# Performance work log

Hardware: AMD Instinct MI355X
Metric: run time of the kernel (lower is better)

## Reference

```python
import jax, jax.numpy as jnp
import numpy as np

HEAD_DIM = 64
NUM_FEATURES = 256


def _sample_orf(head_dim, num_features, seed=0):
    """Orthogonal random features with chi(d)-norm row scaling (FAVOR+)."""
    rng = np.random.RandomState(seed)
    blocks = []
    while len(blocks) * head_dim < num_features:
        G = rng.randn(head_dim, head_dim).astype(np.float32)
        Q, _ = np.linalg.qr(G)
        norms = np.linalg.norm(rng.randn(head_dim, head_dim).astype(np.float32), axis=1)
        blocks.append(np.diag(norms) @ Q.T)
    return np.concatenate(blocks, axis=0)[:num_features].astype(np.float32)


def _phi(x, omega, is_query):
    """FAVOR+ positive feature map with max-subtraction stabilization."""
    m = omega.shape[0]
    proj = jnp.einsum('bhnd,md->bhnm', x, omega)          # [B,H,N,M]
    norm = 0.5 * jnp.sum(x * x, axis=-1, keepdims=True)    # [B,H,N,1]
    log_phi = proj - norm
    if is_query:
        log_phi = log_phi - jnp.max(log_phi, axis=-1, keepdims=True)
    else:
        log_phi = log_phi - jnp.max(log_phi)
    return jnp.exp(log_phi) / np.float32(np.sqrt(m)) + 1e-4


def _causal_scan(phi_q, phi_k, v):
    """Causal linear-attention recurrence via lax.scan. States: S[B,H,M,D], z[B,H,M]."""
    B, H, N, M = phi_q.shape
    D = v.shape[-1]
    # seq-first for scan: [N,B,H,*]
    pq = jnp.moveaxis(phi_q, 2, 0)
    pk = jnp.moveaxis(phi_k, 2, 0)
    vt = jnp.moveaxis(v, 2, 0)

    S0 = jnp.zeros((B, H, M, D), dtype=phi_q.dtype)
    z0 = jnp.zeros((B, H, M), dtype=phi_q.dtype)

    def step(carry, xs):
        S, z = carry
        pq_i, pk_i, v_i = xs  # [B,H,M], [B,H,M], [B,H,D]
        S = S + pk_i[..., :, None] * v_i[..., None, :]
        z = z + pk_i
        num = jnp.einsum('bhm,bhmd->bhd', pq_i, S)
        den = jnp.sum(pq_i * z, axis=-1, keepdims=True) + 1e-6
        return (S, z), num / den

    _, out = jax.lax.scan(step, (S0, z0), (pq, pk, vt))  # out: [N,B,H,D]
    return jnp.moveaxis(out, 0, 2)


def setup_inputs() -> dict:
    key = jax.random.key(0)
    k1, k2, k3 = jax.random.split(key, 3)
    B, H, N, D = 2, 16, 4096, HEAD_DIM
    q = jax.random.normal(k1, (B, H, N, D), dtype=jnp.float32)
    k = jax.random.normal(k2, (B, H, N, D), dtype=jnp.float32)
    v = jax.random.normal(k3, (B, H, N, D), dtype=jnp.float32)
    omega = jnp.asarray(_sample_orf(HEAD_DIM, NUM_FEATURES))
    return {"q": q, "k": k, "v": v, "omega": omega}


def reference(q, k, v, omega):
    scale = q.shape[-1] ** (-0.25)
    phi_q = _phi(q * scale, omega, is_query=True)
    phi_k = _phi(k * scale, omega, is_query=False)
    # q_len == kv_len -> causal scan branch (matches original forward)
    out = _causal_scan(phi_q.astype(jnp.float32), phi_k.astype(jnp.float32),
                       v.astype(jnp.float32))
    return out.astype(q.dtype)
```

## Files before the change

### kernel.cpp

```cpp
#include <hip/hip_runtime.h>
#include <cstddef>

#define BH    32
#define NSEQ  4096
#define MFEAT 256
#define CHUNK 128
#define NCH   32
#define SROW  65
#define SPITCH (SROW*256)

#define SCALE 0.35355339059327373f

typedef unsigned int uint_t;
typedef _Float16 half_t;
typedef __attribute__((ext_vector_type(8))) _Float16 half8;
typedef __attribute__((ext_vector_type(4))) float f32x4;

__device__ __forceinline__ f32x4 mfma16(half8 a, half8 b, f32x4 c) {
  return __builtin_amdgcn_mfma_f32_16x16x32_f16(a, b, c, 0, 0, 0);
}
__device__ __forceinline__ uint_t enc_f(float x) {
  uint_t u = __float_as_uint(x);
  return (u & 0x80000000u) ? ~u : (u | 0x80000000u);
}
__device__ __forceinline__ float dec_f(uint_t u) {
  u = (u & 0x80000000u) ? (u ^ 0x80000000u) : ~u;
  return __uint_as_float(u);
}
__device__ __forceinline__ half8 cvt_h8(float4 a, float4 b) {
  half8 h;
  h[0] = (half_t)a.x; h[1] = (half_t)a.y; h[2] = (half_t)a.z; h[3] = (half_t)a.w;
  h[4] = (half_t)b.x; h[5] = (half_t)b.y; h[6] = (half_t)b.z; h[7] = (half_t)b.w;
  return h;
}

__global__ void k_init(uint_t* kmax) { *kmax = enc_f(-__builtin_inff()); }

__global__ __launch_bounds__(256, 2) void k_maxes(
    const float* __restrict__ q, const float* __restrict__ kx,
    const float* __restrict__ omega, float* __restrict__ rowmQ,
    uint_t* __restrict__ kmax)
{
  __shared__ half_t Wl[256 * 72];
  __shared__ half_t xs[64 * 72];
  __shared__ float nrm[64];
  __shared__ float red[4];

  const int tid = threadIdx.x;
  const int lane = tid & 63;
  const int w = tid >> 6;
  const int lc = lane & 15, rg = lane >> 4, koff = rg * 8;
  const size_t rowbase = (size_t)blockIdx.x * 64;

  for (int l = tid; l < 4096; l += 256) {
    int m = l >> 4, d4 = (l & 15) * 4;
    float4 o = *(const float4*)(omega + m * 64 + d4);
    half_t* p = &Wl[m * 72 + d4];
    p[0] = (half_t)o.x; p[1] = (half_t)o.y; p[2] = (half_t)o.z; p[3] = (half_t)o.w;
  }
  {
    int r = tid >> 2, qd = tid & 3;
    #pragma unroll
    for (int c = 0; c < 4; c++) {
      float4 xv = *(const float4*)(q + (rowbase + r) * 64 + qd * 16 + c * 4);
      half_t* p = &xs[r * 72 + qd * 16 + c * 4];
      p[0] = (half_t)(xv.x * SCALE); p[1] = (half_t)(xv.y * SCALE);
      p[2] = (half_t)(xv.z * SCALE); p[3] = (half_t)(xv.w * SCALE);
    }
  }
  __syncthreads();
  {
    f32x4 acc[16];
    #pragma unroll
    for (int ct = 0; ct < 16; ct++) acc[ct] = (f32x4){0.f, 0.f, 0.f, 0.f};
    #pragma unroll
    for (int ks = 0; ks < 2; ks++) {
      half8 a = *(const half8*)&xs[(w * 16 + lc) * 72 + ks * 32 + koff];
      #pragma unroll
      for (int ct = 0; ct < 16; ct++) {
        half8 b = *(const half8*)&Wl[(ct * 16 + lc) * 72 + ks * 32 + koff];
        acc[ct] = mfma16(a, b, acc[ct]);
      }
    }
    #pragma unroll
    for (int r = 0; r < 4; r++) {
      float m0 = -3.4e38f;
      #pragma unroll
      for (int ct = 0; ct < 16; ct++) m0 = fmaxf(m0, acc[ct][r]);
      m0 = fmaxf(m0, __shfl_xor(m0, 1, 64));
      m0 = fmaxf(m0, __shfl_xor(m0, 2, 64));
      m0 = fmaxf(m0, __shfl_xor(m0, 4, 64));
      m0 = fmaxf(m0, __shfl_xor(m0, 8, 64));
      if (lc == 0) rowmQ[rowbase + w * 16 + rg * 4 + r] = m0;
    }
  }
  __syncthreads();
  {
    int r = tid >> 2, qd = tid & 3;
    float pn = 0.f;
    #pragma unroll
    for (int c = 0; c < 4; c++) {
      float4 xv = *(const float4*)(kx + (rowbase + r) * 64 + qd * 16 + c * 4);
      xv.x *= SCALE; xv.y *= SCALE; xv.z *= SCALE; xv.w *= SCALE;
      pn += xv.x * xv.x + xv.y * xv.y + xv.z * xv.z + xv.w * xv.w;
      half_t* p = &xs[r * 72 + qd * 16 + c * 4];
      p[0] = (half_t)xv.x; p[1] = (half_t)xv.y; p[2] = (half_t)xv.z; p[3] = (half_t)xv.w;
    }
    pn += __shfl_xor(pn, 1, 64);
    pn += __shfl_xor(pn, 2, 64);
    if ((tid & 3) == 0) nrm[r] = 0.5f * pn;
  }
  __syncthreads();
  {
    f32x4 acc[16];
    #pragma unroll
    for (int ct = 0; ct < 16; ct++) acc[ct] = (f32x4){0.f, 0.f, 0.f, 0.f};
    #pragma unroll
    for (int ks = 0; ks < 2; ks++) {
      half8 a = *(const half8*)&xs[(w * 16 + lc) * 72 + ks * 32 + koff];
      #pragma unroll
      for (int ct = 0; ct < 16; ct++) {
        half8 b = *(const half8*)&Wl[(ct * 16 + lc) * 72 + ks * 32 + koff];
        acc[ct] = mfma16(a, b, acc[ct]);
      }
    }
    float hn[4];
    #pragma unroll
    for (int r = 0; r < 4; r++) hn[r] = nrm[w * 16 + rg * 4 + r];
    float bm = -3.4e38f;
    #pragma unroll
    for (int ct = 0; ct < 16; ct++)
      #pragma unroll
      for (int r = 0; r < 4; r++) bm = fmaxf(bm, acc[ct][r] - hn[r]);
    #pragma unroll
    for (int off = 1; off < 64; off <<= 1) bm = fmaxf(bm, __shfl_xor(bm, off, 64));
    if (lane == 0) red[w] = bm;
    __syncthreads();
    if (tid == 0)
      atomicMax(kmax, enc_f(fmaxf(fmaxf(red[0], red[1]), fmaxf(red[2], red[3]))));
  }
}

__global__ __launch_bounds__(256, 2) void k_state(
    const float* __restrict__ kx, const float* __restrict__ v,
    const float* __restrict__ omega, const uint_t* __restrict__ kmax,
    half_t* __restrict__ spA)
{
  __shared__ half_t WP[256 * 72];
  __shared__ half_t vt[80 * 136];
  __shared__ float nrmK[128];

  const int tid = threadIdx.x;
  const int lane = tid & 63;
  const int w = tid >> 6;
  const int lc = lane & 15, rg = lane >> 4, koff = rg * 8;
  const int wr = w * 32;
  const int blk = blockIdx.x;
  const size_t nbase = (size_t)(blk >> 5) * NSEQ + (size_t)(blk & 31) * CHUNK;
  const float gmaxv = dec_f(*kmax);

  for (int l = tid; l < 4096; l += 256) {
    int m = l >> 4, d4 = (l & 15) * 4;
    float4 o = *(const float4*)(omega + m * 64 + d4);
    half_t* p = &WP[m * 72 + d4];
    p[0] = (half_t)o.x; p[1] = (half_t)o.y; p[2] = (half_t)o.z; p[3] = (half_t)o.w;
  }
  for (int l = tid; l < 2048; l += 256) {
    int j = l >> 4, dq = (l & 15) * 4;
    float4 vv = *(const float4*)(v + (nbase + j) * 64 + dq);
    vt[(dq + 0) * 136 + j] = (half_t)vv.x;
    vt[(dq + 1) * 136 + j] = (half_t)vv.y;
    vt[(dq + 2) * 136 + j] = (half_t)vv.z;
    vt[(dq + 3) * 136 + j] = (half_t)vv.w;
  }
  if (tid < 128) vt[64 * 136 + tid] = (half_t)1.0f;

  half8 ak[2][2];
  float pn[2] = {0.f, 0.f};
  #pragma unroll
  for (int rt = 0; rt < 2; rt++) {
    const float* kp = kx + (nbase + wr + rt * 16 + lc) * 64 + koff;
    #pragma unroll
    for (int ks = 0; ks < 2; ks++) {
      float4 a = *(const float4*)(kp + ks * 32);
      float4 b = *(const float4*)(kp + ks * 32 + 4);
      a.x *= SCALE; a.y *= SCALE; a.z *= SCALE; a.w *= SCALE;
      b.x *= SCALE; b.y *= SCALE; b.z *= SCALE; b.w *= SCALE;
      pn[rt] += a.x * a.x + a.y * a.y + a.z * a.z + a.w * a.w
              + b.x * b.x + b.y * b.y + b.z * b.z + b.w * b.w;
      ak[rt][ks] = cvt_h8(a, b);
    }
    pn[rt] += __shfl_xor(pn[rt], 16, 64);
    pn[rt] += __shfl_xor(pn[rt], 32, 64);
  }
  if (rg == 0) {
    nrmK[wr + lc] = 0.5f * pn[0];
    nrmK[wr + 16 + lc] = 0.5f * pn[1];
  }
  __syncthreads();

  f32x4 accP[2][16];
  #pragma unroll
  for (int rt = 0; rt < 2; rt++)
    #pragma unroll
    for (int ct = 0; ct < 16; ct++) accP[rt][ct] = (f32x4){0.f, 0.f, 0.f, 0.f};
  #pragma unroll
  for (int ks = 0; ks < 2; ks++)
    #pragma unroll
    for (int ct = 0; ct < 16; ct++) {
      half8 b = *(const half8*)&WP[(ct * 16 + lc) * 72 + ks * 32 + koff];
      accP[0][ct] = mfma16(ak[0][ks], b, accP[0][ct]);
      accP[1][ct] = mfma16(ak[1][ks], b, accP[1][ct]);
    }
  float hnr[2][4];
  #pragma unroll
  for (int rt = 0; rt < 2; rt++)
    #pragma unroll
    for (int r = 0; r < 4; r++) hnr[rt][r] = nrmK[wr + rt * 16 + rg * 4 + r];
  #pragma unroll
  for (int rt = 0; rt < 2; rt++)
    #pragma unroll
    for (int ct = 0; ct < 16; ct++)
      #pragma unroll
      for (int r = 0; r < 4; r++)
        accP[rt][ct][r] = __expf(accP[rt][ct][r] - hnr[rt][r] - gmaxv) * 0.0625f + 1e-4f;

  half_t* pkT = WP;
  #pragma unroll
  for (int h = 0; h < 2; h++) {
    __syncthreads();
    #pragma unroll
    for (int rt = 0; rt < 2; rt++)
      #pragma unroll
      for (int c8 = 0; c8 < 8; c8++) {
        int ct = h * 8 + c8;
        #pragma unroll
        for (int r = 0; r < 4; r++)
          pkT[(c8 * 16 + lc) * 144 + wr + rt * 16 + rg * 4 + r] = (half_t)accP[rt][ct][r];
      }
    __syncthreads();
    f32x4 acc2[5][2];
    #pragma unroll
    for (int rt = 0; rt < 5; rt++) {
      acc2[rt][0] = (f32x4){0.f, 0.f, 0.f, 0.f};
      acc2[rt][1] = (f32x4){0.f, 0.f, 0.f, 0.f};
    }
    #pragma unroll
    for (int ks = 0; ks < 4; ks++) {
      half8 b0 = *(const half8*)&pkT[((2 * w + 0) * 16 + lc) * 144 + ks * 32 + koff];
      half8 b1 = *(const half8*)&pkT[((2 * w + 1) * 16 + lc) * 144 + ks * 32 + koff];
      #pragma unroll
      for (int rt = 0; rt < 5; rt++) {
        half8 a = *(const half8*)&vt[(rt * 16 + lc) * 136 + ks * 32 + koff];
        acc2[rt][0] = mfma16(a, b0, acc2[rt][0]);
        acc2[rt][1] = mfma16(a, b1, acc2[rt][1]);
      }
    }
    #pragma unroll
    for (int rt = 0; rt < 5; rt++)
      #pragma unroll
      for (int c2 = 0; c2 < 2; c2++)
        #pragma unroll
        for (int r = 0; r < 4; r++) {
          int row = rt * 16 + rg * 4 + r;
          if (row < SROW)
            spA[(size_t)blk * SPITCH + row * 256 + h * 128 + (2 * w + c2) * 16 + lc] =
                (half_t)acc2[rt][c2][r];
        }
  }
}

__global__ __launch_bounds__(256) void k_prefix(
    const uint_t* __restrict__ spA, uint_t* __restrict__ spB)
{
  int r = blockIdx.x * 256 + threadIdx.x;
  if (r >= SPITCH / 2) return;
  int bh = blockIdx.y;
  const uint_t* src = spA + (size_t)bh * NCH * (SPITCH / 2) + r;
  uint_t* dst = spB + (size_t)bh * NCH * (SPITCH / 2) + r;
  float r0 = 0.f, r1 = 0.f;
  for (int c = 0; c < NCH; c++) {
    union { uint_t u; half_t h[2]; } cv, ov;
    cv.u = src[(size_t)c * (SPITCH / 2)];
    ov.h[0] = (half_t)r0; ov.h[1] = (half_t)r1;
    dst[(size_t)c * (SPITCH / 2)] = ov.u;
    r0 += (float)cv.h[0];
    r1 += (float)cv.h[1];
  }
}

__global__ __launch_bounds__(256, 2) void k_attn2(
    const float* __restrict__ q, const float* __restrict__ kx,
    const float* __restrict__ v, const float* __restrict__ omega,
    const float* __restrict__ rowmQ, const uint_t* __restrict__ kmax,
    const half_t* __restrict__ spB, float* __restrict__ out)
{
  __shared__ half_t sm[24192];
  __shared__ float nrmK[128];
  half_t* PQ  = sm;
  half_t* PK  = sm + 9216;
  half_t* SST = sm + 18432;
  half_t* AS  = sm;
  half_t* VT  = sm + 9216;

  const int tid = threadIdx.x;
  const int lane = tid & 63;
  const int w = tid >> 6;
  const int lc = lane & 15, rg = lane >> 4, koff = rg * 8;
  const int wr = w * 32;
  const int blk = blockIdx.x;
  const size_t nbase = (size_t)(blk >> 5) * NSEQ + (size_t)(blk & 31) * CHUNK;
  const half_t* spb = spB + (size_t)blk * SPITCH;
  const float gmaxv = dec_f(*kmax);

  float rowm[2][4];
  #pragma unroll
  for (int rt = 0; rt < 2; rt++)
    #pragma unroll
    for (int r = 0; r < 4; r++)
      rowm[rt][r] = rowmQ[nbase + wr + rt * 16 + rg * 4 + r];

  half8 aq[2][2], ak[2][2];
  float pn[2] = {0.f, 0.f};
  #pragma unroll
  for (int rt = 0; rt < 2; rt++) {
    const float* qp = q + (nbase + wr + rt * 16 + lc) * 64 + koff;
    const float* kp = kx + (nbase + wr + rt * 16 + lc) * 64 + koff;
    #pragma unroll
    for (int ks = 0; ks < 2; ks++) {
      float4 a = *(const float4*)(qp + ks * 32);
      float4 b = *(const float4*)(qp + ks * 32 + 4);
      a.x *= SCALE; a.y *= SCALE; a.z *= SCALE; a.w *= SCALE;
      b.x *= SCALE; b.y *= SCALE; b.z *= SCALE; b.w *= SCALE;
      aq[rt][ks] = cvt_h8(a, b);
      float4 c = *(const float4*)(kp + ks * 32);
      float4 d = *(const float4*)(kp + ks * 32 + 4);
      c.x *= SCALE; c.y *= SCALE; c.z *= SCALE; c.w *= SCALE;
      d.x *= SCALE; d.y *= SCALE; d.z *= SCALE; d.w *= SCALE;
      pn[rt] += c.x * c.x + c.y * c.y + c.z * c.z + c.w * c.w
              + d.x * d.x + d.y * d.y + d.z * d.z + d.w * d.w;
      ak[rt][ks] = cvt_h8(c, d);
    }
    pn[rt] += __shfl_xor(pn[rt], 16, 64);
    pn[rt] += __shfl_xor(pn[rt], 32, 64);
  }
  if (rg == 0) {
    nrmK[wr + lc] = 0.5f * pn[0];
    nrmK[wr + 16 + lc] = 0.5f * pn[1];
  }
  __syncthreads();
  float hnr[2][4];
  #pragma unroll
  for (int rt = 0; rt < 2; rt++)
    #pragma unroll
    for (int r = 0; r < 4; r++) hnr[rt][r] = nrmK[wr + rt * 16 + rg * 4 + r];

  f32x4 accA[2][8], accO[2][5];
  #pragma unroll
  for (int rt = 0; rt < 2; rt++) {
    #pragma unroll
    for (int ct = 0; ct < 8; ct++) accA[rt][ct] = (f32x4){0.f, 0.f, 0.f, 0.f};
    #pragma unroll
    for (int cs = 0; cs < 5; cs++) accO[rt][cs] = (f32x4){0.f, 0.f, 0.f, 0.f};
  }

  for (int mt = 0; mt < 4; mt++) {
    __syncthreads();
    for (int l = tid; l < 520; l += 256) {
      int row = l >> 3, c8 = (l & 7) * 8;
      *(half8*)&SST[row * 72 + c8] = *(const half8*)(spb + row * 256 + mt * 64 + c8);
    }
    half8 bw[4][2];
    #pragma unroll
    for (int ct = 0; ct < 4; ct++) {
      const float* op = omega + (mt * 64 + ct * 16 + lc) * 64 + koff;
      #pragma unroll
      for (int ks = 0; ks < 2; ks++) {
        float4 a = *(const float4*)(op + ks * 32);
        float4 b = *(const float4*)(op + ks * 32 + 4);
        bw[ct][ks] = cvt_h8(a, b);
      }
    }
    f32x4 accP[2][4];
    #pragma unroll
    for (int rt = 0; rt < 2; rt++)
      #pragma unroll
      for (int ct = 0; ct < 4; ct++) accP[rt][ct] = (f32x4){0.f, 0.f, 0.f, 0.f};
    #pragma unroll
    for (int ks = 0; ks < 2; ks++)
      #pragma unroll
      for (int ct = 0; ct < 4; ct++) {
        accP[0][ct] = mfma16(aq[0][ks], bw[ct][ks], accP[0][ct]);
        accP[1][ct] = mfma16(aq[1][ks], bw[ct][ks], accP[1][ct]);
      }
    #pragma unroll
    for (int rt = 0; rt < 2; rt++)
      #pragma unroll
      for (int ct = 0; ct < 4; ct++)
        #pragma unroll
        for (int r = 0; r < 4; r++) {
          float val = __expf(accP[rt][ct][r] - rowm[rt][r]) * 0.0625f + 1e-4f;
          PQ[(wr + rt * 16 + rg * 4 + r) * 72 + ct * 16 + lc] = (half_t)val;
        }
    #pragma unroll
    for (int rt = 0; rt < 2; rt++)
      #pragma unroll
      for (int ct = 0; ct < 4; ct++) accP[rt][ct] = (f32x4){0.f, 0.f, 0.f, 0.f};
    #pragma unroll
    for (int ks = 0; ks < 2; ks++)
      #pragma unroll
      for (int ct = 0; ct < 4; ct++) {
        accP[0][ct] = mfma16(ak[0][ks], bw[ct][ks], accP[0][ct]);
        accP[1][ct] = mfma16(ak[1][ks], bw[ct][ks], accP[1][ct]);
      }
    #pragma unroll
    for (int rt = 0; rt < 2; rt++)
      #pragma unroll
      for (int ct = 0; ct < 4; ct++)
        #pragma unroll
        for (int r = 0; r < 4; r++) {
          float val = __expf(accP[rt][ct][r] - hnr[rt][r] - gmaxv) * 0.0625f + 1e-4f;
          PK[(wr + rt * 16 + rg * 4 + r) * 72 + ct * 16 + lc] = (half_t)val;
        }
    __syncthreads();
    #pragma unroll
    for (int ks2 = 0; ks2 < 64; ks2 += 32) {
      half8 a0 = *(const half8*)&PQ[(wr + lc) * 72 + ks2 + koff];
      half8 a1 = *(const half8*)&PQ[(wr + 16 + lc) * 72 + ks2 + koff];
      #pragma unroll
      for (int ct = 0; ct < 8; ct++) {
        half8 b = *(const half8*)&PK[(ct * 16 + lc) * 72 + ks2 + koff];
        accA[0][ct] = mfma16(a0, b, accA[0][ct]);
        accA[1][ct] = mfma16(a1, b, accA[1][ct]);
      }
      #pragma unroll
      for (int cs = 0; cs < 5; cs++) {
        half8 b = *(const half8*)&SST[(cs * 16 + lc) * 72 + ks2 + koff];
        accO[0][cs] = mfma16(a0, b, accO[0][cs]);
        accO[1][cs] = mfma16(a1, b, accO[1][cs]);
      }
    }
  }

  __syncthreads();
  for (int l = tid; l < 2048; l += 256) {
    int j = l >> 4, dq = (l & 15) * 4;
    float4 vv = *(const float4*)(v + (nbase + j) * 64 + dq);
    VT[(dq + 0) * 136 + j] = (half_t)vv.x;
    VT[(dq + 1) * 136 + j] = (half_t)vv.y;
    VT[(dq + 2) * 136 + j] = (half_t)vv.z;
    VT[(dq + 3) * 136 + j] = (half_t)vv.w;
  }
  if (tid < 128) VT[64 * 136 + tid] = (half_t)1.0f;

  #pragma unroll
  for (int h = 0; h < 2; h++) {
    #pragma unroll
    for (int rt = 0; rt < 2; rt++)
      #pragma unroll
      for (int c4 = 0; c4 < 4; c4++) {
        int ct = h * 4 + c4;
        int j = ct * 16 + lc;
        #pragma unroll
        for (int r = 0; r < 4; r++) {
          int i = wr + rt * 16 + rg * 4 + r;
          float val = (j <= i) ? accA[rt][ct][r] : 0.f;
          AS[i * 72 + (j - h * 64)] = (half_t)val;
        }
      }
    if (h == 0) __syncthreads();
    #pragma unroll
    for (int ks2 = 0; ks2 < 64; ks2 += 32) {
      half8 a0 = *(const half8*)&AS[(wr + lc) * 72 + ks2 + koff];
      half8 a1 = *(const half8*)&AS[(wr + 16 + lc) * 72 + ks2 + koff];
      #pragma unroll
      for (int cs = 0; cs < 5; cs++) {
        half8 b = *(const half8*)&VT[(cs * 16 + lc) * 136 + h * 64 + ks2 + koff];
        accO[0][cs] = mfma16(a0, b, accO[0][cs]);
        accO[1][cs] = mfma16(a1, b, accO[1][cs]);
      }
    }
  }

  #pragma unroll
  for (int rt = 0; rt < 2; rt++)
    #pragma unroll
    for (int r = 0; r < 4; r++) {
      float den = __shfl(accO[rt][4][r], (lane & 48), 64) + 1e-6f;
      float inv = 1.0f / den;
      int i = wr + rt * 16 + rg * 4 + r;
      #pragma unroll
      for (int cs = 0; cs < 4; cs++)
        out[(nbase + i) * 64 + cs * 16 + lc] = accO[rt][cs][r] * inv;
    }
}

extern "C" void kernel_launch(void* const* d_in, const int* in_sizes, int n_in,
                              void* d_out, int out_size, void* d_ws, size_t ws_size,
                              hipStream_t stream) {
  const float* q = (const float*)d_in[0];
  const float* k = (const float*)d_in[1];
  const float* v = (const float*)d_in[2];
  const float* omega = (const float*)d_in[3];
  float* out = (float*)d_out;
  char* ws = (char*)d_ws;

  float*  rowmQ = (float*)(ws + 0);
  half_t* spA   = (half_t*)(ws + 524288);
  half_t* spB   = (half_t*)(ws + 34603008);
  uint_t* kmax  = (uint_t*)(ws + 68681728);

  k_init<<<1, 1, 0, stream>>>(kmax);
  k_maxes<<<2048, 256, 0, stream>>>(q, k, omega, rowmQ, kmax);
  k_state<<<1024, 256, 0, stream>>>(k, v, omega, kmax, spA);
  k_prefix<<<dim3(33, 32), 256, 0, stream>>>((const uint_t*)spA, (uint_t*)spB);
  k_attn2<<<1024, 256, 0, stream>>>(q, k, v, omega, rowmQ, kmax, spB, out);
}
```

Measured before the change: 157.4 us.

## Pipeline attention stages with register prefetch, XOR-swizzled LDS and staged output stores

In k_maxes, q and k rows now load straight into MFMA registers instead of going through shared memory, which removes a staging buffer and a barrier and lets the occupancy hint rise. In the attention kernel, the omega and state tiles for the next feature block are prefetched into registers while the current block computes, and the V tile is loaded early. Padded LDS rows are replaced by XOR-swizzled 64-wide rows so the blocks use less shared memory, and the occupancy hint goes to 3. The output is staged through LDS and written as coalesced float4 stores. The extra prefetch registers could cause spills under the higher occupancy target.

```diff
diff --git a/kernel.cpp b/kernel.cpp
--- a/kernel.cpp
+++ b/kernel.cpp
@@ -36,13 +36,12 @@
 
 __global__ void k_init(uint_t* kmax) { *kmax = enc_f(-__builtin_inff()); }
 
-__global__ __launch_bounds__(256, 2) void k_maxes(
+__global__ __launch_bounds__(256, 4) void k_maxes(
     const float* __restrict__ q, const float* __restrict__ kx,
     const float* __restrict__ omega, float* __restrict__ rowmQ,
     uint_t* __restrict__ kmax)
 {
   __shared__ half_t Wl[256 * 72];
-  __shared__ half_t xs[64 * 72];
   __shared__ float nrm[64];
   __shared__ float red[4];
 
@@ -58,87 +57,87 @@
     half_t* p = &Wl[m * 72 + d4];
     p[0] = (half_t)o.x; p[1] = (half_t)o.y; p[2] = (half_t)o.z; p[3] = (half_t)o.w;
   }
+  half8 aq[2], akf[2];
   {
-    int r = tid >> 2, qd = tid & 3;
-    #pragma unroll
-    for (int c = 0; c < 4; c++) {
-      float4 xv = *(const float4*)(q + (rowbase + r) * 64 + qd * 16 + c * 4);
-      half_t* p = &xs[r * 72 + qd * 16 + c * 4];
-      p[0] = (half_t)(xv.x * SCALE); p[1] = (half_t)(xv.y * SCALE);
-      p[2] = (half_t)(xv.z * SCALE); p[3] = (half_t)(xv.w * SCALE);
-    }
-  }
-  __syncthreads();
-  {
-    f32x4 acc[16];
-    #pragma unroll
-    for (int ct = 0; ct < 16; ct++) acc[ct] = (f32x4){0.f, 0.f, 0.f, 0.f};
+    const float* qp = q + (rowbase + w * 16 + lc) * 64 + koff;
+    const float* kp = kx + (rowbase + w * 16 + lc) * 64 + koff;
+    float pn = 0.f;
     #pragma unroll
     for (int ks = 0; ks < 2; ks++) {
-      half8 a = *(const half8*)&xs[(w * 16 + lc) * 72 + ks * 32 + koff];
-      #pragma unroll
-      for (int ct = 0; ct < 16; ct++) {
-        half8 b = *(const half8*)&Wl[(ct * 16 + lc) * 72 + ks * 32 + koff];
-        acc[ct] = mfma16(a, b, acc[ct]);
+      float4 a = *(const float4*)(qp + ks * 32);
+      float4 b = *(const float4*)(qp + ks * 32 + 4);
+      a.x *= SCALE; a.y *= SCALE; a.z *= SCALE; a.w *= SCALE;
+      b.x *= SCALE; b.y *= SCALE; b.z *= SCALE; b.w *= SCALE;
+      aq[ks] = cvt_h8(a, b);
+      float4 c = *(const float4*)(kp + ks * 32);
+      float4 d = *(const float4*)(kp + ks * 32 + 4);
+      c.x *= SCALE; c.y *= SCALE; c.z *= SCALE; c.w *= SCALE;
+      d.x *= SCALE; d.y *= SCALE; d.z *= SCALE; d.w *= SCALE;
+      pn += c.x * c.x + c.y * c.y + c.z * c.z + c.w * c.w
+          + d.x * d.x + d.y * d.y + d.z * d.z + d.w * d.w;
+      akf[ks] = cvt_h8(c, d);
+    }
+    pn += __shfl_xor(pn, 16, 64);
+    pn += __shfl_xor(pn, 32, 64);
+    if (rg == 0) nrm[w * 16 + lc] = 0.5f * pn;
+  }
+  __syncthreads();
+
+  float mrow[4] = {-3.4e38f, -3.4e38f, -3.4e38f, -3.4e38f};
+  #pragma unroll
+  for (int hh = 0; hh < 2; hh++) {
+    f32x4 acc[8];
+    #pragma unroll
+    for (int c = 0; c < 8; c++) acc[c] = (f32x4){0.f, 0.f, 0.f, 0.f};
+    #pragma unroll
+    for (int ks = 0; ks < 2; ks++)
+      #pragma unroll
+      for (int c = 0; c < 8; c++) {
+        half8 b = *(const half8*)&Wl[((hh * 8 + c) * 16 + lc) * 72 + ks * 32 + koff];
+        acc[c] = mfma16(aq[ks], b, acc[c]);
       }
-    }
-    #pragma unroll
-    for (int r = 0; r < 4; r++) {
-      float m0 = -3.4e38f;
-      #pragma unroll
-      for (int ct = 0; ct < 16; ct++) m0 = fmaxf(m0, acc[ct][r]);
-      m0 = fmaxf(m0, __shfl_xor(m0, 1, 64));
-      m0 = fmaxf(m0, __shfl_xor(m0, 2, 64));
-      m0 = fmaxf(m0, __shfl_xor(m0, 4, 64));
-      m0 = fmaxf(m0, __shfl_xor(m0, 8, 64));
-      if (lc == 0) rowmQ[rowbase + w * 16 + rg * 4 + r] = m0;
-    }
-  }
-  __syncthreads();
-  {
-    int r = tid >> 2, qd = tid & 3;
-    float pn = 0.f;
-    #pragma unroll
-    for (int c = 0; c < 4; c++) {
-      float4 xv = *(const float4*)(kx + (rowbase + r) * 64 + qd * 16 + c * 4);
-      xv.x *= SCALE; xv.y *= SCALE; xv.z *= SCALE; xv.w *= SCALE;
-      pn += xv.x * xv.x + xv.y * xv.y + xv.z * xv.z + xv.w * xv.w;
-      half_t* p = &xs[r * 72 + qd * 16 + c * 4];
-      p[0] = (half_t)xv.x; p[1] = (half_t)xv.y; p[2] = (half_t)xv.z; p[3] = (half_t)xv.w;
-    }
-    pn += __shfl_xor(pn, 1, 64);
-    pn += __shfl_xor(pn, 2, 64);
-    if ((tid & 3) == 0) nrm[r] = 0.5f * pn;
-  }
-  __syncthreads();
-  {
-    f32x4 acc[16];
-    #pragma unroll
-    for (int ct = 0; ct < 16; ct++) acc[ct] = (f32x4){0.f, 0.f, 0.f, 0.f};
-    #pragma unroll
-    for (int ks = 0; ks < 2; ks++) {
-      half8 a = *(const half8*)&xs[(w * 16 + lc) * 72 + ks * 32 + koff];
-      #pragma unroll
-      for (int ct = 0; ct < 16; ct++) {
-        half8 b = *(const half8*)&Wl[(ct * 16 + lc) * 72 + ks * 32 + koff];
-        acc[ct] = mfma16(a, b, acc[ct]);
+    #pragma unroll
+    for (int c = 0; c < 8; c++)
+      #pragma unroll
+      for (int r = 0; r < 4; r++) mrow[r] = fmaxf(mrow[r], acc[c][r]);
+  }
+  #pragma unroll
+  for (int r = 0; r < 4; r++) {
+    float m0 = mrow[r];
+    m0 = fmaxf(m0, __shfl_xor(m0, 1, 64));
+    m0 = fmaxf(m0, __shfl_xor(m0, 2, 64));
+    m0 = fmaxf(m0, __shfl_xor(m0, 4, 64));
+    m0 = fmaxf(m0, __shfl_xor(m0, 8, 64));
+    if (lc == 0) rowmQ[rowbase + w * 16 + rg * 4 + r] = m0;
+  }
+
+  float hn[4];
+  #pragma unroll
+  for (int r = 0; r < 4; r++) hn[r] = nrm[w * 16 + rg * 4 + r];
+  float bm = -3.4e38f;
+  #pragma unroll
+  for (int hh = 0; hh < 2; hh++) {
+    f32x4 acc[8];
+    #pragma unroll
+    for (int c = 0; c < 8; c++) acc[c] = (f32x4){0.f, 0.f, 0.f, 0.f};
+    #pragma unroll
+    for (int ks = 0; ks < 2; ks++)
+      #pragma unroll
+      for (int c = 0; c < 8; c++) {
+        half8 b = *(const half8*)&Wl[((hh * 8 + c) * 16 + lc) * 72 + ks * 32 + koff];
+        acc[c] = mfma16(akf[ks], b, acc[c]);
       }
-    }
-    float hn[4];
-    #pragma unroll
-    for (int r = 0; r < 4; r++) hn[r] = nrm[w * 16 + rg * 4 + r];
-    float bm = -3.4e38f;
-    #pragma unroll
-    for (int ct = 0; ct < 16; ct++)
-      #pragma unroll
-      for (int r = 0; r < 4; r++) bm = fmaxf(bm, acc[ct][r] - hn[r]);
-    #pragma unroll
-    for (int off = 1; off < 64; off <<= 1) bm = fmaxf(bm, __shfl_xor(bm, off, 64));
-    if (lane == 0) red[w] = bm;
-    __syncthreads();
-    if (tid == 0)
-      atomicMax(kmax, enc_f(fmaxf(fmaxf(red[0], red[1]), fmaxf(red[2], red[3]))));
-  }
+    #pragma unroll
+    for (int c = 0; c < 8; c++)
+      #pragma unroll
+      for (int r = 0; r < 4; r++) bm = fmaxf(bm, acc[c][r] - hn[r]);
+  }
+  #pragma unroll
+  for (int off = 1; off < 64; off <<= 1) bm = fmaxf(bm, __shfl_xor(bm, off, 64));
+  if (lane == 0) red[w] = bm;
+  __syncthreads();
+  if (tid == 0)
+    atomicMax(kmax, enc_f(fmaxf(fmaxf(red[0], red[1]), fmaxf(red[2], red[3]))));
 }
 
 __global__ __launch_bounds__(256, 2) void k_state(
@@ -289,19 +288,19 @@
   }
 }
 
-__global__ __launch_bounds__(256, 2) void k_attn2(
+__global__ __launch_bounds__(256, 3) void k_attn3(
     const float* __restrict__ q, const float* __restrict__ kx,
     const float* __restrict__ v, const float* __restrict__ omega,
     const float* __restrict__ rowmQ, const uint_t* __restrict__ kmax,
     const half_t* __restrict__ spB, float* __restrict__ out)
 {
-  __shared__ half_t sm[24192];
+  __shared__ half_t sm[21504];
   __shared__ float nrmK[128];
   half_t* PQ  = sm;
-  half_t* PK  = sm + 9216;
-  half_t* SST = sm + 18432;
+  half_t* PK  = sm + 8192;
+  half_t* SST = sm + 16384;
   half_t* AS  = sm;
-  half_t* VT  = sm + 9216;
+  half_t* VT  = sm + 8192;
 
   const int tid = threadIdx.x;
   const int lane = tid & 63;
@@ -312,6 +311,7 @@
   const size_t nbase = (size_t)(blk >> 5) * NSEQ + (size_t)(blk & 31) * CHUNK;
   const half_t* spb = spB + (size_t)blk * SPITCH;
   const float gmaxv = dec_f(*kmax);
+  const int swz = (lc & 7) << 3;
 
   float rowm[2][4];
   #pragma unroll
@@ -348,6 +348,89 @@
     nrmK[wr + lc] = 0.5f * pn[0];
     nrmK[wr + 16 + lc] = 0.5f * pn[1];
   }
+
+  half8 bw0[4][2], bw1[4][2];
+  half8 sstA, sstB, sstC = half8{};
+
+#define LOADW(BW, MT) do {                                                    \
+    _Pragma("unroll") for (int ct = 0; ct < 4; ct++) {                        \
+      const float* op = omega + ((MT) * 64 + ct * 16 + lc) * 64 + koff;       \
+      float4 a0_ = *(const float4*)(op);                                      \
+      float4 b0_ = *(const float4*)(op + 4);                                  \
+      float4 a1_ = *(const float4*)(op + 32);                                 \
+      float4 b1_ = *(const float4*)(op + 36);                                 \
+      BW[ct][0] = cvt_h8(a0_, b0_);                                          \
+      BW[ct][1] = cvt_h8(a1_, b1_);                                          \
+    } } while (0)
+
+#define LOADSST(MT) do {                                                      \
+    { int l = tid;       int ro = l >> 3, c8 = (l & 7) * 8;                   \
+      sstA = *(const half8*)(spb + ro * 256 + (MT) * 64 + c8); }              \
+    { int l = tid + 256; int ro = l >> 3, c8 = (l & 7) * 8;                   \
+      sstB = *(const half8*)(spb + ro * 256 + (MT) * 64 + c8); }              \
+    if (tid < 8) { int l = tid + 512; int ro = l >> 3, c8 = (l & 7) * 8;      \
+      sstC = *(const half8*)(spb + ro * 256 + (MT) * 64 + c8); }              \
+  } while (0)
+
+#define STAGEPHASE(BW) do {                                                   \
+    { int l = tid;       int ro = l >> 3, c8 = (l & 7) * 8;                   \
+      *(half8*)&SST[ro * 64 + (c8 ^ ((ro & 7) << 3))] = sstA; }               \
+    { int l = tid + 256; int ro = l >> 3, c8 = (l & 7) * 8;                   \
+      *(half8*)&SST[ro * 64 + (c8 ^ ((ro & 7) << 3))] = sstB; }               \
+    if (tid < 8) { int l = tid + 512; int ro = l >> 3, c8 = (l & 7) * 8;      \
+      *(half8*)&SST[ro * 64 + (c8 ^ ((ro & 7) << 3))] = sstC; }               \
+    f32x4 accP[2][4];                                                         \
+    _Pragma("unroll") for (int rt = 0; rt < 2; rt++)                          \
+      _Pragma("unroll") for (int ct = 0; ct < 4; ct++)                        \
+        accP[rt][ct] = (f32x4){0.f, 0.f, 0.f, 0.f};                           \
+    _Pragma("unroll") for (int ks = 0; ks < 2; ks++)                          \
+      _Pragma("unroll") for (int ct = 0; ct < 4; ct++) {                      \
+        accP[0][ct] = mfma16(aq[0][ks], BW[ct][ks], accP[0][ct]);             \
+        accP[1][ct] = mfma16(aq[1][ks], BW[ct][ks], accP[1][ct]);             \
+      }                                                                       \
+    _Pragma("unroll") for (int rt = 0; rt < 2; rt++)                          \
+      _Pragma("unroll") for (int ct = 0; ct < 4; ct++)                        \
+        _Pragma("unroll") for (int r = 0; r < 4; r++) {                       \
+          int i = wr + rt * 16 + rg * 4 + r;                                  \
+          float val = __expf(accP[rt][ct][r] - rowm[rt][r]) * 0.0625f + 1e-4f;\
+          PQ[i * 64 + ((ct * 16 + lc) ^ ((i & 7) << 3))] = (half_t)val;       \
+        }                                                                     \
+    _Pragma("unroll") for (int rt = 0; rt < 2; rt++)                          \
+      _Pragma("unroll") for (int ct = 0; ct < 4; ct++)                        \
+        accP[rt][ct] = (f32x4){0.f, 0.f, 0.f, 0.f};                           \
+    _Pragma("unroll") for (int ks = 0; ks < 2; ks++)                          \
+      _Pragma("unroll") for (int ct = 0; ct < 4; ct++) {                      \
+        accP[0][ct] = mfma16(ak[0][ks], BW[ct][ks], accP[0][ct]);             \
+        accP[1][ct] = mfma16(ak[1][ks], BW[ct][ks], accP[1][ct]);             \
+      }                                                                       \
+    _Pragma("unroll") for (int rt = 0; rt < 2; rt++)                          \
+      _Pragma("unroll") for (int ct = 0; ct < 4; ct++)                        \
+        _Pragma("unroll") for (int r = 0; r < 4; r++) {                       \
+          int i = wr + rt * 16 + rg * 4 + r;                                  \
+          float val = __expf(accP[rt][ct][r] - hnr[rt][r] - gmaxv) * 0.0625f + 1e-4f; \
+          PK[i * 64 + ((ct * 16 + lc) ^ ((i & 7) << 3))] = (half_t)val;       \
+        }                                                                     \
+  } while (0)
+
+#define COMPUTEPHASE() do {                                                   \
+    _Pragma("unroll") for (int ks2 = 0; ks2 < 64; ks2 += 32) {                \
+      int sA = (ks2 + koff) ^ swz;                                            \
+      half8 a0 = *(const half8*)&PQ[(wr + lc) * 64 + sA];                     \
+      half8 a1 = *(const half8*)&PQ[(wr + 16 + lc) * 64 + sA];                \
+      _Pragma("unroll") for (int ct = 0; ct < 8; ct++) {                      \
+        half8 b = *(const half8*)&PK[(ct * 16 + lc) * 64 + sA];               \
+        accA[0][ct] = mfma16(a0, b, accA[0][ct]);                             \
+        accA[1][ct] = mfma16(a1, b, accA[1][ct]);                             \
+      }                                                                       \
+      _Pragma("unroll") for (int cs = 0; cs < 5; cs++) {                      \
+        half8 b = *(const half8*)&SST[(cs * 16 + lc) * 64 + sA];              \
+        accO[0][cs] = mfma16(a0, b, accO[0][cs]);                             \
+        accO[1][cs] = mfma16(a1, b, accO[1][cs]);                             \
+      }                                                                       \
+    } } while (0)
+
+  LOADW(bw0, 0);
+  LOADSST(0);
   __syncthreads();
   float hnr[2][4];
   #pragma unroll
@@ -364,94 +447,49 @@
     for (int cs = 0; cs < 5; cs++) accO[rt][cs] = (f32x4){0.f, 0.f, 0.f, 0.f};
   }
 
-  for (int mt = 0; mt < 4; mt++) {
-    __syncthreads();
-    for (int l = tid; l < 520; l += 256) {
-      int row = l >> 3, c8 = (l & 7) * 8;
-      *(half8*)&SST[row * 72 + c8] = *(const half8*)(spb + row * 256 + mt * 64 + c8);
-    }
-    half8 bw[4][2];
-    #pragma unroll
-    for (int ct = 0; ct < 4; ct++) {
-      const float* op = omega + (mt * 64 + ct * 16 + lc) * 64 + koff;
-      #pragma unroll
-      for (int ks = 0; ks < 2; ks++) {
-        float4 a = *(const float4*)(op + ks * 32);
-        float4 b = *(const float4*)(op + ks * 32 + 4);
-        bw[ct][ks] = cvt_h8(a, b);
-      }
-    }
-    f32x4 accP[2][4];
-    #pragma unroll
-    for (int rt = 0; rt < 2; rt++)
-      #pragma unroll
-      for (int ct = 0; ct < 4; ct++) accP[rt][ct] = (f32x4){0.f, 0.f, 0.f, 0.f};
-    #pragma unroll
-    for (int ks = 0; ks < 2; ks++)
-      #pragma unroll
-      for (int ct = 0; ct < 4; ct++) {
-        accP[0][ct] = mfma16(aq[0][ks], bw[ct][ks], accP[0][ct]);
-        accP[1][ct] = mfma16(aq[1][ks], bw[ct][ks], accP[1][ct]);
-      }
-    #pragma unroll
-    for (int rt = 0; rt < 2; rt++)
-      #pragma unroll
-      for (int ct = 0; ct < 4; ct++)
-        #pragma unroll
-        for (int r = 0; r < 4; r++) {
-          float val = __expf(accP[rt][ct][r] - rowm[rt][r]) * 0.0625f + 1e-4f;
-          PQ[(wr + rt * 16 + rg * 4 + r) * 72 + ct * 16 + lc] = (half_t)val;
-        }
-    #pragma unroll
-    for (int rt = 0; rt < 2; rt++)
-      #pragma unroll
-      for (int ct = 0; ct < 4; ct++) accP[rt][ct] = (f32x4){0.f, 0.f, 0.f, 0.f};
-    #pragma unroll
-    for (int ks = 0; ks < 2; ks++)
-      #pragma unroll
-      for (int ct = 0; ct < 4; ct++) {
-        accP[0][ct] = mfma16(ak[0][ks], bw[ct][ks], accP[0][ct]);
-        accP[1][ct] = mfma16(ak[1][ks], bw[ct][ks], accP[1][ct]);
-      }
-    #pragma unroll
-    for (int rt = 0; rt < 2; rt++)
-      #pragma unroll
-      for (int ct = 0; ct < 4; ct++)
-        #pragma unroll
-        for (int r = 0; r < 4; r++) {
-          float val = __expf(accP[rt][ct][r] - hnr[rt][r] - gmaxv) * 0.0625f + 1e-4f;
-          PK[(wr + rt * 16 + rg * 4 + r) * 72 + ct * 16 + lc] = (half_t)val;
-        }
-    __syncthreads();
-    #pragma unroll
-    for (int ks2 = 0; ks2 < 64; ks2 += 32) {
-      half8 a0 = *(const half8*)&PQ[(wr + lc) * 72 + ks2 + koff];
-      half8 a1 = *(const half8*)&PQ[(wr + 16 + lc) * 72 + ks2 + koff];
-      #pragma unroll
-      for (int ct = 0; ct < 8; ct++) {
-        half8 b = *(const half8*)&PK[(ct * 16 + lc) * 72 + ks2 + koff];
-        accA[0][ct] = mfma16(a0, b, accA[0][ct]);
-        accA[1][ct] = mfma16(a1, b, accA[1][ct]);
-      }
-      #pragma unroll
-      for (int cs = 0; cs < 5; cs++) {
-        half8 b = *(const half8*)&SST[(cs * 16 + lc) * 72 + ks2 + koff];
-        accO[0][cs] = mfma16(a0, b, accO[0][cs]);
-        accO[1][cs] = mfma16(a1, b, accO[1][cs]);
-      }
-    }
-  }
-
-  __syncthreads();
-  for (int l = tid; l < 2048; l += 256) {
-    int j = l >> 4, dq = (l & 15) * 4;
-    float4 vv = *(const float4*)(v + (nbase + j) * 64 + dq);
-    VT[(dq + 0) * 136 + j] = (half_t)vv.x;
-    VT[(dq + 1) * 136 + j] = (half_t)vv.y;
-    VT[(dq + 2) * 136 + j] = (half_t)vv.z;
-    VT[(dq + 3) * 136 + j] = (half_t)vv.w;
-  }
-  if (tid < 128) VT[64 * 136 + tid] = (half_t)1.0f;
+  float4 vv0, vv1, vv2, vv3, vv4, vv5, vv6, vv7;
+
+  STAGEPHASE(bw0);
+  __syncthreads();
+  LOADW(bw1, 1); LOADSST(1);
+  COMPUTEPHASE();
+  __syncthreads();
+  STAGEPHASE(bw1);
+  __syncthreads();
+  LOADW(bw0, 2); LOADSST(2);
+  COMPUTEPHASE();
+  __syncthreads();
+  STAGEPHASE(bw0);
+  __syncthreads();
+  LOADW(bw1, 3); LOADSST(3);
+  COMPUTEPHASE();
+  __syncthreads();
+  STAGEPHASE(bw1);
+  __syncthreads();
+  {
+    const float* vb = v + nbase * 64;
+    vv0 = *(const float4*)(vb + ((tid + 0 * 256) >> 4) * 64 + ((tid + 0 * 256) & 15) * 4);
+    vv1 = *(const float4*)(vb + ((tid + 1 * 256) >> 4) * 64 + ((tid + 1 * 256) & 15) * 4);
+    vv2 = *(const float4*)(vb + ((tid + 2 * 256) >> 4) * 64 + ((tid + 2 * 256) & 15) * 4);
+    vv3 = *(const float4*)(vb + ((tid + 3 * 256) >> 4) * 64 + ((tid + 3 * 256) & 15) * 4);
+    vv4 = *(const float4*)(vb + ((tid + 4 * 256) >> 4) * 64 + ((tid + 4 * 256) & 15) * 4);
+    vv5 = *(const float4*)(vb + ((tid + 5 * 256) >> 4) * 64 + ((tid + 5 * 256) & 15) * 4);
+    vv6 = *(const float4*)(vb + ((tid + 6 * 256) >> 4) * 64 + ((tid + 6 * 256) & 15) * 4);
+    vv7 = *(const float4*)(vb + ((tid + 7 * 256) >> 4) * 64 + ((tid + 7 * 256) & 15) * 4);
+  }
+  COMPUTEPHASE();
+  __syncthreads();
+
+#define PUTV(VV, E) do {                                                      \
+    int l = tid + (E) * 256; int j = l >> 4, dq = (l & 15) * 4;               \
+    VT[(dq + 0) * 128 + (j ^ (((dq + 0) & 7) << 3))] = (half_t)VV.x;          \
+    VT[(dq + 1) * 128 + (j ^ (((dq + 1) & 7) << 3))] = (half_t)VV.y;          \
+    VT[(dq + 2) * 128 + (j ^ (((dq + 2) & 7) << 3))] = (half_t)VV.z;          \
+    VT[(dq + 3) * 128 + (j ^ (((dq + 3) & 7) << 3))] = (half_t)VV.w;          \
+  } while (0)
+  PUTV(vv0, 0); PUTV(vv1, 1); PUTV(vv2, 2); PUTV(vv3, 3);
+  PUTV(vv4, 4); PUTV(vv5, 5); PUTV(vv6, 6); PUTV(vv7, 7);
+  if (tid < 128) VT[64 * 128 + tid] = (half_t)1.0f;
 
   #pragma unroll
   for (int h = 0; h < 2; h++) {
@@ -465,23 +503,27 @@
         for (int r = 0; r < 4; r++) {
           int i = wr + rt * 16 + rg * 4 + r;
           float val = (j <= i) ? accA[rt][ct][r] : 0.f;
-          AS[i * 72 + (j - h * 64)] = (half_t)val;
+          AS[i * 64 + ((j - h * 64) ^ ((i & 7) << 3))] = (half_t)val;
         }
       }
     if (h == 0) __syncthreads();
     #pragma unroll
     for (int ks2 = 0; ks2 < 64; ks2 += 32) {
-      half8 a0 = *(const half8*)&AS[(wr + lc) * 72 + ks2 + koff];
-      half8 a1 = *(const half8*)&AS[(wr + 16 + lc) * 72 + ks2 + koff];
+      int sA = (ks2 + koff) ^ swz;
+      int sV = (h * 64 + ks2 + koff) ^ swz;
+      half8 a0 = *(const half8*)&AS[(wr + lc) * 64 + sA];
+      half8 a1 = *(const half8*)&AS[(wr + 16 + lc) * 64 + sA];
       #pragma unroll
       for (int cs = 0; cs < 5; cs++) {
-        half8 b = *(const half8*)&VT[(cs * 16 + lc) * 136 + h * 64 + ks2 + koff];
+        half8 b = *(const half8*)&VT[(cs * 16 + lc) * 128 + sV];
         accO[0][cs] = mfma16(a0, b, accO[0][cs]);
         accO[1][cs] = mfma16(a1, b, accO[1][cs]);
       }
     }
   }
 
+  __syncthreads();
+  float* OS = (float*)sm;
   #pragma unroll
   for (int rt = 0; rt < 2; rt++)
     #pragma unroll
@@ -491,8 +533,21 @@
       int i = wr + rt * 16 + rg * 4 + r;
       #pragma unroll
       for (int cs = 0; cs < 4; cs++)
-        out[(nbase + i) * 64 + cs * 16 + lc] = accO[rt][cs][r] * inv;
-    }
+        OS[i * 68 + cs * 16 + lc] = accO[rt][cs][r] * inv;
+    }
+  __syncthreads();
+  #pragma unroll
+  for (int e = 0; e < 8; e++) {
+    int l = tid + e * 256;
+    int row = l >> 4, c4 = (l & 15) * 4;
+    float4 t4 = *(const float4*)&OS[row * 68 + c4];
+    *(float4*)(out + (nbase + row) * 64 + c4) = t4;
+  }
+#undef LOADW
+#undef LOADSST
+#undef STAGEPHASE
+#undef COMPUTEPHASE
+#undef PUTV
 }
 
 extern "C" void kernel_launch(void* const* d_in, const int* in_sizes, int n_in,
@@ -514,5 +569,5 @@
   k_maxes<<<2048, 256, 0, stream>>>(q, k, omega, rowmQ, kmax);
   k_state<<<1024, 256, 0, stream>>>(k, v, omega, kmax, spA);
   k_prefix<<<dim3(33, 32), 256, 0, stream>>>((const uint_t*)spA, (uint_t*)spB);
-  k_attn2<<<1024, 256, 0, stream>>>(q, k, v, omega, rowmQ, kmax, spB, out);
-}
+  k_attn3<<<1024, 256, 0, stream>>>(q, k, v, omega, rowmQ, kmax, spB, out);
+}
```

After: 389.2 us. 2.47x slower.
